# Kernel tuning notes

Measured on AMD Instinct MI355X. Metric: run time of the kernel, lower is better.

Reference implementation:

```python
import jax, jax.numpy as jnp
import numpy as np

B, S, N, H, W = 2, 8192, 512, 480, 640
NUM_CLASSES = 10
IMG_MEAN = np.array([103.53, 116.28, 123.675], dtype=np.float32)


def _depth_to_cam(p, Rt):
    # DEPTH (x right, y forward, z up) -> CAM (x right, y down, z forward)
    q = p @ Rt.T
    return jnp.stack([q[..., 0], -q[..., 2], q[..., 1]], axis=-1)


def _cam_to_depth(c, Rt):
    q = jnp.stack([c[..., 0], c[..., 2], -c[..., 1]], axis=-1)
    return q @ Rt


def setup_inputs() -> dict:
    key = jax.random.key(0)
    k1, k2, k3, k4, k5, k6 = jax.random.split(key, 6)
    mean = jnp.asarray(IMG_MEAN)
    # normalized image: raw pixel minus per-channel mean (so (img+mean-128)/128 is in [-1,1])
    img = jax.random.uniform(k1, (B, 3, H, W), jnp.float32) * 255.0 - mean[None, :, None, None]
    # seeds in DEPTH coords: x right, y forward (positive depth), z up
    u = jax.random.uniform(k2, (B, S, 3), jnp.float32)
    seeds = jnp.stack([(u[..., 0] - 0.5) * 4.0, u[..., 1] * 4.0 + 1.0, (u[..., 2] - 0.5) * 2.0], axis=-1)
    cx = jax.random.uniform(k3, (B, N), jnp.float32) * (W - 1)
    cy = jax.random.uniform(k4, (B, N), jnp.float32) * (H - 1)
    wh = jax.random.uniform(k5, (B, N, 2), jnp.float32) * 120.0 + 20.0
    l = jnp.clip(cx - wh[..., 0] / 2, 0.0, W - 1.0)
    r = jnp.clip(cx + wh[..., 0] / 2, 0.0, W - 1.0)
    t = jnp.clip(cy - wh[..., 1] / 2, 0.0, H - 1.0)
    b = jnp.clip(cy + wh[..., 1] / 2, 0.0, H - 1.0)
    conf = jax.random.uniform(k6, (B, N), jnp.float32)
    cls = jax.random.randint(jax.random.fold_in(key, 7), (B, N), 0, NUM_CLASSES).astype(jnp.float32)
    bboxes_2d = jnp.stack([l, t, r, b, conf, cls], axis=-1)  # [B,N,6]
    Rt = jnp.broadcast_to(jnp.eye(3, dtype=jnp.float32), (B, 3, 3))
    K = jnp.broadcast_to(
        jnp.array([[530.0, 0.0, W / 2], [0.0, 530.0, H / 2], [0.0, 0.0, 1.0]], jnp.float32), (B, 3, 3))
    return {"img": img, "bboxes_2d": bboxes_2d, "seeds_3d": seeds, "Rt": Rt, "K": K}


def _per_sample(img, bbox, seeds, Rt, K):
    mean = jnp.asarray(IMG_MEAN)
    f_u, f_v = K[0, 0], K[1, 1]
    cam = _depth_to_cam(seeds, Rt)                       # [S,3] seeds in camera frame
    uv = cam @ K.T
    seed_2d = uv[:, :2] / uv[:, 2:3]                     # [S,2] projected seeds
    sx = jnp.clip(seed_2d[:, 0], 0.0, W - 1.0)
    sy = jnp.clip(seed_2d[:, 1], 0.0, H - 1.0)
    idx = jnp.floor(sy).astype(jnp.int32) * W + jnp.floor(sx).astype(jnp.int32)  # flat pixel index
    # texture cue: gather raw pixels at seed locations, renormalized to [-1,1]
    flat = ((img.reshape(3, -1) + mean[:, None]) - 128.0) / 128.0
    txt = flat[:, idx].T                                  # [S,3]
    l, t, r, b, conf, cls = (bbox[:, j] for j in range(6))
    midx = (l + r) * 0.5
    midy = (t + b) * 0.5
    sxe = seed_2d[:, 0:1]
    sye = seed_2d[:, 1:2]
    in_box = (sxe > l) & (sxe < r) & (sye > t) & (sye < b)    # [S,N]
    # semantic cue: scatter conf into class slot == one_hot * conf
    sem = jax.nn.one_hot(cls.astype(jnp.int32), NUM_CLASSES, dtype=jnp.float32) * conf[:, None]  # [N,C]
    du = midx[None, :] - sxe                              # [S,N]
    dv = midy[None, :] - sye
    x3, y3, z3 = cam[:, 0:1], cam[:, 1:2], cam[:, 2:3]
    geo0 = du * (z3 / f_u)
    geo1 = dv * (z3 / f_v)
    geo_xy = _cam_to_depth(jnp.stack([geo0, geo1, jnp.zeros_like(geo0)], axis=-1), Rt)  # [S,N,3]
    seed_depth = seeds[:, 1:2]                            # depth-frame forward axis
    ratio = seed_depth / (seed_depth + geo_xy[..., 1])
    geo_xy = geo_xy * ratio[..., None]
    geo_vec = _cam_to_depth(
        jnp.stack([geo0 + x3, geo1 + y3, jnp.broadcast_to(z3, geo0.shape)], axis=-1), Rt)
    geo_vec = geo_vec / jnp.linalg.norm(geo_vec, axis=-1, keepdims=True)
    geo_cue = jnp.concatenate([geo_xy[..., jnp.array([0, 2])], geo_vec], axis=-1)  # [S,N,5]
    asgn = jnp.argmin(du * du + dv * dv, axis=1)          # nearest-center bbox per seed
    pos_geo = jnp.take_along_axis(geo_cue, asgn[:, None, None], axis=1)[:, 0]      # [S,5]
    pos = jnp.concatenate([sem[asgn], txt, pos_geo], axis=-1)                      # [S,18]
    valid = in_box.sum(axis=1) > 0
    return jnp.where(valid[:, None], pos, 0.0).T          # [18,S]


def reference(img, bboxes_2d, seeds_3d, Rt, K):
    return jax.vmap(_per_sample)(img, bboxes_2d, seeds_3d, Rt, K)  # [B,18,S]
```

## Files before the change

### kernel.cpp

```cpp
#include <hip/hip_runtime.h>
#include <math.h>

#define WID 640
#define HEI 480
#define HW (WID * HEI)
#define SEEDS 8192
#define NBOX 512
#define NFEAT 18
#define TPS 32
#define SPB 8

__global__ __launch_bounds__(256) void votefusion_kernel(
    const float* __restrict__ img,
    const float* __restrict__ bb,
    const float* __restrict__ seeds,
    const float* __restrict__ Rt,
    const float* __restrict__ Km,
    float* __restrict__ out)
{
    const int b   = blockIdx.y;
    const int tid = threadIdx.x;
    const int grp = tid >> 5;
    const int t   = tid & 31;
    const int s   = blockIdx.x * SPB + grp;

    const float* bbB = bb + (size_t)b * NBOX * 6;

    const float* R  = Rt + (size_t)b * 9;
    const float* Ko = Km + (size_t)b * 9;
    const float R00 = R[0], R01 = R[1], R02 = R[2];
    const float R10 = R[3], R11 = R[4], R12 = R[5];
    const float R20 = R[6], R21 = R[7], R22 = R[8];
    const float K00 = Ko[0], K01 = Ko[1], K02 = Ko[2];
    const float K10 = Ko[3], K11 = Ko[4], K12 = Ko[5];
    const float K20 = Ko[6], K21 = Ko[7], K22 = Ko[8];

    const float* sp = seeds + ((size_t)b * SEEDS + s) * 3;
    const float s0 = sp[0], s1 = sp[1], s2 = sp[2];
    const float q0 = R00 * s0 + R01 * s1 + R02 * s2;
    const float q1 = R10 * s0 + R11 * s1 + R12 * s2;
    const float q2 = R20 * s0 + R21 * s1 + R22 * s2;
    const float cam0 = q0, cam1 = -q2, cam2 = q1;
    const float uv0 = K00 * cam0 + K01 * cam1 + K02 * cam2;
    const float uv1 = K10 * cam0 + K11 * cam1 + K12 * cam2;
    const float uv2 = K20 * cam0 + K21 * cam1 + K22 * cam2;
    const float sxe = uv0 / uv2;
    const float sye = uv1 / uv2;

    unsigned long long key = 0xFFFFFFFFFFFFFFFFull;
    int any = 0;
    #pragma unroll
    for (int i = 0; i < NBOX / TPS; ++i) {
        const int j = i * TPS + t;
        const float2 lt = *(const float2*)(bbB + j * 6);
        const float2 rb = *(const float2*)(bbB + j * 6 + 2);
        const float midx = __fmul_rn(__fadd_rn(lt.x, rb.x), 0.5f);
        const float midy = __fmul_rn(__fadd_rn(lt.y, rb.y), 0.5f);
        const float du = __fsub_rn(midx, sxe);
        const float dv = __fsub_rn(midy, sye);
        const float d2 = __fadd_rn(__fmul_rn(du, du), __fmul_rn(dv, dv));
        const unsigned long long k =
            ((unsigned long long)__float_as_uint(d2) << 32) | (unsigned)j;
        key = (k < key) ? k : key;
        any |= (sxe > lt.x) & (sxe < rb.x) & (sye > lt.y) & (sye < rb.y);
    }

    #pragma unroll
    for (int m = 1; m < TPS; m <<= 1) {
        const unsigned long long ok = __shfl_xor(key, m);
        key = (ok < key) ? ok : key;
    }
    {
        const unsigned long long bal = __ballot(any != 0);
        any = ((unsigned)(bal >> (tid & 32)) != 0u);
    }

    const int bi = (int)(unsigned)(key & 0xFFFFFFFFull);

    float val = 0.0f;
    if (any && t < NFEAT) {
        if (t < 10) {
            const float conf = bbB[bi * 6 + 4];
            const int   cls  = (int)bbB[bi * 6 + 5];
            val = (t == cls) ? conf : 0.0f;
        } else if (t < 13) {
            const float sx = fminf(fmaxf(sxe, 0.0f), (float)(WID - 1));
            const float sy = fminf(fmaxf(sye, 0.0f), (float)(HEI - 1));
            const int ix = (int)floorf(sx);
            const int iy = (int)floorf(sy);
            const int pidx = iy * WID + ix;
            const float mc = (t == 10) ? 103.53f : (t == 11) ? 116.28f : 123.675f;
            const float* imgB = img + (size_t)b * 3 * HW;
            val = ((imgB[(t - 10) * HW + pidx] + mc) - 128.0f) * (1.0f / 128.0f);
        } else {
            const float2 lt = *(const float2*)(bbB + bi * 6);
            const float2 rb = *(const float2*)(bbB + bi * 6 + 2);
            const float midx = __fmul_rn(__fadd_rn(lt.x, rb.x), 0.5f);
            const float midy = __fmul_rn(__fadd_rn(lt.y, rb.y), 0.5f);
            const float du = midx - sxe;
            const float dv = midy - sye;
            const float x3 = cam0, y3 = cam1, z3 = cam2;
            const float geo0 = du * (z3 / K00);
            const float geo1 = dv * (z3 / K11);

            const float gxy0 = geo0 * R00 - geo1 * R20;
            const float gxy1 = geo0 * R01 - geo1 * R21;
            const float gxy2 = geo0 * R02 - geo1 * R22;
            const float ratio = s1 / (s1 + gxy1);
            const float gx = gxy0 * ratio;
            const float gz = gxy2 * ratio;

            const float a0 = geo0 + x3;
            const float a1 = z3;
            const float a2 = -(geo1 + y3);
            const float gv0 = a0 * R00 + a1 * R10 + a2 * R20;
            const float gv1 = a0 * R01 + a1 * R11 + a2 * R21;
            const float gv2 = a0 * R02 + a1 * R12 + a2 * R22;
            const float inr = 1.0f / sqrtf(gv0 * gv0 + gv1 * gv1 + gv2 * gv2);
            val = (t == 13) ? gx
                : (t == 14) ? gz
                : (t == 15) ? gv0 * inr
                : (t == 16) ? gv1 * inr
                :             gv2 * inr;
        }
    }

    if (t < NFEAT) {
        const size_t base = (size_t)b * NFEAT * SEEDS + s;
        out[base + (size_t)t * SEEDS] = val;
    }
}

extern "C" void kernel_launch(void* const* d_in, const int* in_sizes, int n_in,
                              void* d_out, int out_size, void* d_ws, size_t ws_size,
                              hipStream_t stream) {
    const float* img   = (const float*)d_in[0];
    const float* bb    = (const float*)d_in[1];
    const float* seeds = (const float*)d_in[2];
    const float* Rt    = (const float*)d_in[3];
    const float* K     = (const float*)d_in[4];
    float* out = (float*)d_out;

    const int B = in_sizes[1] / (NBOX * 6);
    dim3 grid(SEEDS / SPB, B);
    votefusion_kernel<<<grid, 256, 0, stream>>>(img, bb, seeds, Rt, K, out);
}
```

Measured before the change: 13.23 us.

## Prefetch image texel early, split argmin key, coalesce output via LDS

Moves the image gather for the texture features before the bbox scan so its latency overlaps the argmin loop. Replaces the packed 64-bit argmin key with a separate float/int pair and an explicit tie-break on index, avoiding 64-bit compares and shuffles. Stages the per-seed outputs through shared memory so each feature row is written as 8 contiguous floats instead of scattered single stores. This adds a block barrier and a small LDS buffer, and the image load now happens even for seeds that end up invalid.

```diff
diff --git a/kernel.cpp b/kernel.cpp
--- a/kernel.cpp
+++ b/kernel.cpp
@@ -47,8 +47,17 @@
     const float sxe = uv0 / uv2;
     const float sye = uv1 / uv2;
 
-    unsigned long long key = 0xFFFFFFFFFFFFFFFFull;
-    int any = 0;
+    float tex = 0.0f;
+    if (t >= 10 && t < 13) {
+        const float sx = fminf(fmaxf(sxe, 0.0f), (float)(WID - 1));
+        const float sy = fminf(fmaxf(sye, 0.0f), (float)(HEI - 1));
+        const int pidx = (int)floorf(sy) * WID + (int)floorf(sx);
+        tex = img[(size_t)b * 3 * HW + (size_t)(t - 10) * HW + pidx];
+    }
+
+    float fmin = 3.0e38f;
+    int   jbest = 0;
+    int   any = 0;
     #pragma unroll
     for (int i = 0; i < NBOX / TPS; ++i) {
         const int j = i * TPS + t;
@@ -59,23 +68,26 @@
         const float du = __fsub_rn(midx, sxe);
         const float dv = __fsub_rn(midy, sye);
         const float d2 = __fadd_rn(__fmul_rn(du, du), __fmul_rn(dv, dv));
-        const unsigned long long k =
-            ((unsigned long long)__float_as_uint(d2) << 32) | (unsigned)j;
-        key = (k < key) ? k : key;
+        const bool less = d2 < fmin;
+        fmin  = less ? d2 : fmin;
+        jbest = less ? j  : jbest;
         any |= (sxe > lt.x) & (sxe < rb.x) & (sye > lt.y) & (sye < rb.y);
     }
 
     #pragma unroll
     for (int m = 1; m < TPS; m <<= 1) {
-        const unsigned long long ok = __shfl_xor(key, m);
-        key = (ok < key) ? ok : key;
+        const float of = __shfl_xor(fmin, m);
+        const int   oj = __shfl_xor(jbest, m);
+        const bool take = (of < fmin) | ((of == fmin) & (oj < jbest));
+        fmin  = take ? of : fmin;
+        jbest = take ? oj : jbest;
     }
     {
         const unsigned long long bal = __ballot(any != 0);
         any = ((unsigned)(bal >> (tid & 32)) != 0u);
     }
 
-    const int bi = (int)(unsigned)(key & 0xFFFFFFFFull);
+    const int bi = jbest;
 
     float val = 0.0f;
     if (any && t < NFEAT) {
@@ -84,14 +96,8 @@
             const int   cls  = (int)bbB[bi * 6 + 5];
             val = (t == cls) ? conf : 0.0f;
         } else if (t < 13) {
-            const float sx = fminf(fmaxf(sxe, 0.0f), (float)(WID - 1));
-            const float sy = fminf(fmaxf(sye, 0.0f), (float)(HEI - 1));
-            const int ix = (int)floorf(sx);
-            const int iy = (int)floorf(sy);
-            const int pidx = iy * WID + ix;
             const float mc = (t == 10) ? 103.53f : (t == 11) ? 116.28f : 123.675f;
-            const float* imgB = img + (size_t)b * 3 * HW;
-            val = ((imgB[(t - 10) * HW + pidx] + mc) - 128.0f) * (1.0f / 128.0f);
+            val = ((tex + mc) - 128.0f) * (1.0f / 128.0f);
         } else {
             const float2 lt = *(const float2*)(bbB + bi * 6);
             const float2 rb = *(const float2*)(bbB + bi * 6 + 2);
@@ -125,9 +131,15 @@
         }
     }
 
-    if (t < NFEAT) {
-        const size_t base = (size_t)b * NFEAT * SEEDS + s;
-        out[base + (size_t)t * SEEDS] = val;
+    __shared__ float lds[SPB][NFEAT + 1];
+    if (t < NFEAT) lds[grp][t] = val;
+    __syncthreads();
+
+    if (tid < SPB * NFEAT) {
+        const int f  = tid >> 3;
+        const int sl = tid & 7;
+        const int sbase = blockIdx.x * SPB;
+        out[(size_t)b * NFEAT * SEEDS + (size_t)f * SEEDS + sbase + sl] = lds[sl][f];
     }
 }
 
```

New measurement: 13.62 us. 1.03x slower.
